# Kernel optimization log

Hardware: AMD Instinct MI355X
Metric: run time of the kernel (lower is better)

Reference implementation:

```python
import jax, jax.numpy as jnp
import numpy as np

B, T, N, D = 32, 50, 100, 4
E = N * (N - 1)
N_IN, N_HID, N_OUT = T * D, 256, 4


def _mlp(x, w1, b1, w2, b2):
    # Linear -> ReLU -> (dropout=0) -> Linear
    return jax.nn.relu(x @ w1 + b1) @ w2 + b2


def setup_inputs() -> dict:
    key = jax.random.key(0)
    ks = jax.random.split(key, 12)
    # fully-connected directed graph, no self loops
    idx = np.array([(i, j) for i in range(N) for j in range(N) if i != j], dtype=np.int64)
    recv, sendr = idx[:, 0], idx[:, 1]
    rec = jnp.asarray(np.eye(N, dtype=np.float32)[recv])    # [E, N]
    send = jnp.asarray(np.eye(N, dtype=np.float32)[sendr])  # [E, N]

    def lin(k, fan_in, fan_out):
        kw, kb = jax.random.split(k)
        w = jax.random.normal(kw, (fan_in, fan_out), jnp.float32) * 0.02
        b = jax.random.normal(kb, (fan_out,), jnp.float32) * 0.02
        return w, b

    x = jax.random.normal(ks[0], (B, T, N, D), jnp.float32)
    w1a, b1a = lin(ks[1], N_IN, N_HID)
    w1b, b1b = lin(ks[2], N_HID, N_HID)
    w2a, b2a = lin(ks[3], 2 * N_HID, N_HID)
    w2b, b2b = lin(ks[4], N_HID, N_HID)
    w3a, b3a = lin(ks[5], N_HID, N_HID)
    w3b, b3b = lin(ks[6], N_HID, N_HID)
    w4a, b4a = lin(ks[7], 3 * N_HID, N_HID)
    w4b, b4b = lin(ks[8], N_HID, N_HID)
    wo, bo = lin(ks[9], N_HID, N_OUT)
    return {"x": x, "rec": rec, "send": send,
            "w1a": w1a, "b1a": b1a, "w1b": w1b, "b1b": b1b,
            "w2a": w2a, "b2a": b2a, "w2b": w2b, "b2b": b2b,
            "w3a": w3a, "b3a": b3a, "w3b": w3b, "b3b": b3b,
            "w4a": w4a, "b4a": b4a, "w4b": w4b, "b4b": b4b,
            "wo": wo, "bo": bo}


def reference(x, rec, send,
              w1a, b1a, w1b, b1b,
              w2a, b2a, w2b, b2b,
              w3a, b3a, w3b, b3b,
              w4a, b4a, w4b, b4b,
              wo, bo):
    # [B, T, N, D] -> [B, N, T*D]
    h = jnp.transpose(x, (0, 2, 1, 3)).reshape(x.shape[0], x.shape[2], -1)
    h = _mlp(h, w1a, b1a, w1b, b1b)                       # [B, N, H]
    # v2e: gather receiver/sender node states to edges
    e = jnp.concatenate([jnp.einsum('en,bnh->beh', rec, h),
                         jnp.einsum('en,bnh->beh', send, h)], axis=2)  # [B, E, 2H]
    e = _mlp(e, w2a, b2a, w2b, b2b)                       # [B, E, H]
    x_skip = e
    # e2v: scatter edges back to nodes, normalize by n_nodes
    v = jnp.einsum('en,beh->bnh', rec, e) / e.shape[-2] * (e.shape[-2] / rec.shape[1])
    v = jnp.einsum('en,beh->bnh', rec, e) / rec.shape[1]  # incoming / incoming.size(1)=N
    v = _mlp(v, w3a, b3a, w3b, b3b)                       # [B, N, H]
    e2 = jnp.concatenate([jnp.einsum('en,bnh->beh', rec, v),
                          jnp.einsum('en,bnh->beh', send, v)], axis=2)  # [B, E, 2H]
    e2 = jnp.concatenate([e2, x_skip], axis=2)            # [B, E, 3H]
    e2 = _mlp(e2, w4a, b4a, w4b, b4b)                     # [B, E, H]
    return e2 @ wo + bo                                   # [B, E, n_out]
```

## Files before the change

### kernel.cpp

```cpp
#include <hip/hip_runtime.h>
#include <hip/hip_bf16.h>
#include <stdint.h>


typedef __attribute__((ext_vector_type(8))) short short8;
typedef __attribute__((ext_vector_type(4))) float float4v;
typedef __attribute__((ext_vector_type(4))) unsigned short ushort4v;

__device__ inline float bf2f(unsigned short u) {
    union { unsigned int i; float f; } v; v.i = ((unsigned int)u) << 16; return v.f;
}

#if __has_builtin(__builtin_amdgcn_cvt_pk_bf16_f32)
typedef __attribute__((ext_vector_type(2))) __bf16 bf16x2;
__device__ inline unsigned int f2bf_pk(float a, float b) {
    union { bf16x2 v; unsigned int u; } c;
    c.v = __builtin_amdgcn_cvt_pk_bf16_f32(a, b);
    return c.u;
}
__device__ inline unsigned short f2bf(float f) {
    return (unsigned short)(f2bf_pk(f, f) & 0xFFFFu);
}
#else
__device__ inline unsigned short f2bf(float f) {
    union { float f; unsigned int i; } v; v.f = f;
    unsigned int i = v.i;
    return (unsigned short)((i + 0x7FFFu + ((i >> 16) & 1u)) >> 16);
}
__device__ inline unsigned int f2bf_pk(float a, float b) {
    return (unsigned int)f2bf(a) | ((unsigned int)f2bf(b) << 16);
}
#endif

__global__ __launch_bounds__(256) void prep_kernel(
        const float* __restrict__ x,
        const float* __restrict__ w1a, const float* __restrict__ w1b,
        const float* __restrict__ w2a, const float* __restrict__ w2b,
        const float* __restrict__ w3a, const float* __restrict__ w3b,
        const float* __restrict__ w4a, const float* __restrict__ b4a,
        const float* __restrict__ w4b, const float* __restrict__ b4b,
        const float* __restrict__ wo,  const float* __restrict__ bo,
        const float* __restrict__ b2b,
        unsigned short* __restrict__ Wp1a, unsigned short* __restrict__ Wp1b,
        unsigned short* __restrict__ Wp2r, unsigned short* __restrict__ Wp2s,
        unsigned short* __restrict__ Wp2b, unsigned short* __restrict__ Wp3a,
        unsigned short* __restrict__ Wp3b, unsigned short* __restrict__ Wp4r,
        unsigned short* __restrict__ Wp4s, unsigned short* __restrict__ Wpz,
        unsigned short* __restrict__ Wfp, float* __restrict__ bfv,
        float* __restrict__ b4ap, float* __restrict__ b2bs,
        unsigned short* __restrict__ hin) {
    int bx = blockIdx.x;
    int tid = threadIdx.x;
    if (bx < 2272) {
        const float* W; unsigned short* Wp; int Kin; int b0;
        if      (bx <  224) { W = w1a;             Wp = Wp1a; Kin = 200; b0 = 0;    }
        else if (bx <  480) { W = w1b;             Wp = Wp1b; Kin = 256; b0 = 224;  }
        else if (bx <  736) { W = w2a;             Wp = Wp2r; Kin = 256; b0 = 480;  }
        else if (bx <  992) { W = w2a + 256 * 256; Wp = Wp2s; Kin = 256; b0 = 736;  }
        else if (bx < 1248) { W = w2b;             Wp = Wp2b; Kin = 256; b0 = 992;  }
        else if (bx < 1504) { W = w3a;             Wp = Wp3a; Kin = 256; b0 = 1248; }
        else if (bx < 1760) { W = w3b;             Wp = Wp3b; Kin = 256; b0 = 1504; }
        else if (bx < 2016) { W = w4a;             Wp = Wp4r; Kin = 256; b0 = 1760; }
        else                { W = w4a + 256 * 256; Wp = Wp4s; Kin = 256; b0 = 2016; }
        int idx = (bx - b0) * 256 + tid;
        int k = idx >> 8, n = idx & 255;
        unsigned short v = (k < Kin) ? f2bf(W[k * 256 + n]) : (unsigned short)0;
        Wp[((size_t)(k >> 5) * 256 + n) * 32 + (k & 31)] = v;
    } else if (bx < 2528) {
        int k = bx - 2272, c = tid;
        float s = 0.f;
        for (int t = 0; t < 256; ++t)
            s += w2b[k * 256 + t] * w4a[(size_t)(512 + t) * 256 + c];
        Wpz[((size_t)(k >> 5) * 256 + c) * 32 + (k & 31)] = f2bf(s);
    } else if (bx < 2530) {
        int k = tid;
        if (bx == 2528) {
            float a[4] = {0.f, 0.f, 0.f, 0.f};
            for (int c = 0; c < 256; ++c) {
                float wv = w4b[k * 256 + c];
                #pragma unroll
                for (int o = 0; o < 4; ++o) a[o] += wv * wo[c * 4 + o];
            }
            #pragma unroll
            for (int n = 0; n < 16; ++n)
                Wfp[(size_t)(k >> 5) * 512 + n * 32 + (k & 31)] =
                    (n < 4) ? f2bf(a[n]) : (unsigned short)0;
            if (k < 4) {
                float s = bo[k];
                for (int c = 0; c < 256; ++c) s += b4b[c] * wo[c * 4 + k];
                bfv[k] = s;
            }
        } else {
            float s = b4a[k];
            for (int t = 0; t < 256; ++t)
                s += b2b[t] * w4a[(size_t)(512 + t) * 256 + k];
            b4ap[k] = s;
            b2bs[k] = 0.99f * b2b[k];
        }
    } else {
        int idx = (bx - 2530) * 256 + tid;
        if (idx < 3200 * 224) {
            int row = idx / 224;
            int c = idx - row * 224;
            int b = row / 100, n = row - b * 100;
            unsigned short v = 0;
            if (c < 200) {
                int t = c >> 2, d = c & 3;
                v = f2bf(x[(((size_t)(b * 50 + t)) * 100 + n) * 4 + d]);
            }
            hin[(size_t)row * 224 + c] = v;
        }
    }
}

__global__ __launch_bounds__(256) void node_fusedA_kernel(
        const unsigned short* __restrict__ hin,
        const unsigned short* __restrict__ Wp1a, const float* __restrict__ b1a,
        const unsigned short* __restrict__ Wp1b, const float* __restrict__ b1b,
        const unsigned short* __restrict__ Wp2r, const float* __restrict__ b2a,
        const unsigned short* __restrict__ Wp2s,
        unsigned short* __restrict__ U, unsigned short* __restrict__ Hs) {
    __shared__ __align__(16) unsigned short t1s[16 * 264];
    __shared__ __align__(16) unsigned short hs2[16 * 264];
    const int m0 = blockIdx.x * 16;
    const int tid  = threadIdx.x;
    const int wave = tid >> 6;
    const int lane = tid & 63;
    const int l15  = lane & 15;
    const int quad = lane >> 4;
    const int n0   = wave * 64;
    const int koff = quad * 8;

    {
        float4v acc[4];
        #pragma unroll
        for (int ni = 0; ni < 4; ++ni) acc[ni] = (float4v)(0.0f);
        for (int kb = 0; kb < 7; ++kb) {
            short8 af = *(const short8*)(hin + (size_t)(m0 + l15) * 224 + kb * 32 + koff);
            short8 bf[4];
            #pragma unroll
            for (int ni = 0; ni < 4; ++ni)
                bf[ni] = *(const short8*)(Wp1a + ((size_t)kb * 256 + n0 + ni * 16 + l15) * 32 + koff);
            #pragma unroll
            for (int ni = 0; ni < 4; ++ni)
                acc[ni] = __builtin_amdgcn_mfma_f32_16x16x32_bf16(af, bf[ni], acc[ni], 0, 0, 0);
        }
        #pragma unroll
        for (int ni = 0; ni < 4; ++ni) {
            int col = n0 + ni * 16 + l15;
            float bv = b1a[col];
            #pragma unroll
            for (int r = 0; r < 4; ++r) {
                float v = acc[ni][r] + bv;
                v = v > 0.f ? v : 0.f;
                t1s[(quad * 4 + r) * 264 + col] = f2bf(v);
            }
        }
    }
    __syncthreads();

    {
        float4v acc[4];
        #pragma unroll
        for (int ni = 0; ni < 4; ++ni) acc[ni] = (float4v)(0.0f);
        for (int kb = 0; kb < 8; ++kb) {
            short8 af = *(const short8*)(&t1s[l15 * 264 + kb * 32 + koff]);
            short8 bf[4];
            #pragma unroll
            for (int ni = 0; ni < 4; ++ni)
                bf[ni] = *(const short8*)(Wp1b + ((size_t)kb * 256 + n0 + ni * 16 + l15) * 32 + koff);
            #pragma unroll
            for (int ni = 0; ni < 4; ++ni)
                acc[ni] = __builtin_amdgcn_mfma_f32_16x16x32_bf16(af, bf[ni], acc[ni], 0, 0, 0);
        }
        #pragma unroll
        for (int ni = 0; ni < 4; ++ni) {
            int col = n0 + ni * 16 + l15;
            float bv = b1b[col];
            #pragma unroll
            for (int r = 0; r < 4; ++r)
                hs2[(quad * 4 + r) * 264 + col] = f2bf(acc[ni][r] + bv);
        }
    }
    __syncthreads();

    {
        float4v aU[4], aH[4];
        #pragma unroll
        for (int ni = 0; ni < 4; ++ni) { aU[ni] = (float4v)(0.0f); aH[ni] = (float4v)(0.0f); }
        for (int kb = 0; kb < 8; ++kb) {
            short8 af = *(const short8*)(&hs2[l15 * 264 + kb * 32 + koff]);
            #pragma unroll
            for (int ni = 0; ni < 4; ++ni) {
                short8 bu = *(const short8*)(Wp2r + ((size_t)kb * 256 + n0 + ni * 16 + l15) * 32 + koff);
                short8 bh = *(const short8*)(Wp2s + ((size_t)kb * 256 + n0 + ni * 16 + l15) * 32 + koff);
                aU[ni] = __builtin_amdgcn_mfma_f32_16x16x32_bf16(af, bu, aU[ni], 0, 0, 0);
                aH[ni] = __builtin_amdgcn_mfma_f32_16x16x32_bf16(af, bh, aH[ni], 0, 0, 0);
            }
        }
        #pragma unroll
        for (int ni = 0; ni < 4; ++ni) {
            int col = n0 + ni * 16 + l15;
            float bv = b2a[col];
            #pragma unroll
            for (int r = 0; r < 4; ++r) {
                size_t o = (size_t)(m0 + quad * 4 + r) * 256 + col;
                U[o]  = f2bf(aU[ni][r] + bv);
                Hs[o] = f2bf(aH[ni][r]);
            }
        }
    }
}

__global__ __launch_bounds__(256) void node_fusedC_kernel(
        const unsigned short* __restrict__ Ssc,
        const unsigned short* __restrict__ Wp2b, const float* __restrict__ b2bs,
        const unsigned short* __restrict__ Wp3a, const float* __restrict__ b3a,
        const unsigned short* __restrict__ Wp3b, const float* __restrict__ b3b,
        const unsigned short* __restrict__ Wp4r, const float* __restrict__ b4ap,
        const unsigned short* __restrict__ Wp4s,
        unsigned short* __restrict__ C4, unsigned short* __restrict__ Vs) {
    __shared__ __align__(16) unsigned short buf0[16 * 264];
    __shared__ __align__(16) unsigned short buf1[16 * 264];
    const int m0 = blockIdx.x * 16;
    const int tid  = threadIdx.x;
    const int wave = tid >> 6;
    const int lane = tid & 63;
    const int l15  = lane & 15;
    const int quad = lane >> 4;
    const int n0   = wave * 64;
    const int koff = quad * 8;

    {
        float4v acc[4];
        #pragma unroll
        for (int ni = 0; ni < 4; ++ni) acc[ni] = (float4v)(0.0f);
        for (int kb = 0; kb < 8; ++kb) {
            short8 af = *(const short8*)(Ssc + (size_t)(m0 + l15) * 256 + kb * 32 + koff);
            short8 bf[4];
            #pragma unroll
            for (int ni = 0; ni < 4; ++ni)
                bf[ni] = *(const short8*)(Wp2b + ((size_t)kb * 256 + n0 + ni * 16 + l15) * 32 + koff);
            #pragma unroll
            for (int ni = 0; ni < 4; ++ni)
                acc[ni] = __builtin_amdgcn_mfma_f32_16x16x32_bf16(af, bf[ni], acc[ni], 0, 0, 0);
        }
        #pragma unroll
        for (int ni = 0; ni < 4; ++ni) {
            int col = n0 + ni * 16 + l15;
            float bv = b2bs[col];
            #pragma unroll
            for (int r = 0; r < 4; ++r)
                buf0[(quad * 4 + r) * 264 + col] = f2bf(acc[ni][r] + bv);
        }
    }
    __syncthreads();

    {
        float4v acc[4];
        #pragma unroll
        for (int ni = 0; ni < 4; ++ni) acc[ni] = (float4v)(0.0f);
        for (int kb = 0; kb < 8; ++kb) {
            short8 af = *(const short8*)(&buf0[l15 * 264 + kb * 32 + koff]);
            short8 bf[4];
            #pragma unroll
            for (int ni = 0; ni < 4; ++ni)
                bf[ni] = *(const short8*)(Wp3a + ((size_t)kb * 256 + n0 + ni * 16 + l15) * 32 + koff);
            #pragma unroll
            for (int ni = 0; ni < 4; ++ni)
                acc[ni] = __builtin_amdgcn_mfma_f32_16x16x32_bf16(af, bf[ni], acc[ni], 0, 0, 0);
        }
        #pragma unroll
        for (int ni = 0; ni < 4; ++ni) {
            int col = n0 + ni * 16 + l15;
            float bv = b3a[col];
            #pragma unroll
            for (int r = 0; r < 4; ++r) {
                float v = acc[ni][r] + bv;
                v = v > 0.f ? v : 0.f;
                buf1[(quad * 4 + r) * 264 + col] = f2bf(v);
            }
        }
    }
    __syncthreads();

    {
        float4v acc[4];
        #pragma unroll
        for (int ni = 0; ni < 4; ++ni) acc[ni] = (float4v)(0.0f);
        for (int kb = 0; kb < 8; ++kb) {
            short8 af = *(const short8*)(&buf1[l15 * 264 + kb * 32 + koff]);
            short8 bf[4];
            #pragma unroll
            for (int ni = 0; ni < 4; ++ni)
                bf[ni] = *(const short8*)(Wp3b + ((size_t)kb * 256 + n0 + ni * 16 + l15) * 32 + koff);
            #pragma unroll
            for (int ni = 0; ni < 4; ++ni)
                acc[ni] = __builtin_amdgcn_mfma_f32_16x16x32_bf16(af, bf[ni], acc[ni], 0, 0, 0);
        }
        __syncthreads();
        #pragma unroll
        for (int ni = 0; ni < 4; ++ni) {
            int col = n0 + ni * 16 + l15;
            float bv = b3b[col];
            #pragma unroll
            for (int r = 0; r < 4; ++r)
                buf0[(quad * 4 + r) * 264 + col] = f2bf(acc[ni][r] + bv);
        }
    }
    __syncthreads();

    {
        float4v aC[4], aV[4];
        #pragma unroll
        for (int ni = 0; ni < 4; ++ni) { aC[ni] = (float4v)(0.0f); aV[ni] = (float4v)(0.0f); }
        for (int kb = 0; kb < 8; ++kb) {
            short8 af = *(const short8*)(&buf0[l15 * 264 + kb * 32 + koff]);
            #pragma unroll
            for (int ni = 0; ni < 4; ++ni) {
                short8 bc = *(const short8*)(Wp4r + ((size_t)kb * 256 + n0 + ni * 16 + l15) * 32 + koff);
                short8 bv = *(const short8*)(Wp4s + ((size_t)kb * 256 + n0 + ni * 16 + l15) * 32 + koff);
                aC[ni] = __builtin_amdgcn_mfma_f32_16x16x32_bf16(af, bc, aC[ni], 0, 0, 0);
                aV[ni] = __builtin_amdgcn_mfma_f32_16x16x32_bf16(af, bv, aV[ni], 0, 0, 0);
            }
        }
        #pragma unroll
        for (int ni = 0; ni < 4; ++ni) {
            int col = n0 + ni * 16 + l15;
            float bv = b4ap[col];
            #pragma unroll
            for (int r = 0; r < 4; ++r) {
                size_t o = (size_t)(m0 + quad * 4 + r) * 256 + col;
                C4[o] = f2bf(aC[ni][r] + bv);
                Vs[o] = f2bf(aV[ni][r]);
            }
        }
    }
}

__global__ __launch_bounds__(256) void colsum_kernel(
        const unsigned short* __restrict__ U, const unsigned short* __restrict__ Hs,
        unsigned short* __restrict__ Ssc) {
    const int g = blockIdx.x;
    const int b = g / 100, i = g - b * 100;
    const int c = threadIdx.x;
    const float u = bf2f(U[(size_t)g * 256 + c]);
    const unsigned short* base = Hs + (size_t)b * 100 * 256 + c;
    float s = 0.f;
    #pragma unroll 4
    for (int j = 0; j < 100; ++j) {
        float v = u + bf2f(base[(size_t)j * 256]);
        s += (v > 0.f ? v : 0.f);
    }
    float vi = u + bf2f(base[(size_t)i * 256]);
    s -= (vi > 0.f ? vi : 0.f);
    Ssc[(size_t)g * 256 + c] = f2bf(s * 0.01f);
}

__global__ __launch_bounds__(512, 6) void edge_phaseB_kernel(
        const unsigned short* __restrict__ Hs, const unsigned short* __restrict__ Vs,
        const unsigned short* __restrict__ U, const unsigned short* __restrict__ C4,
        const unsigned short* __restrict__ Wpz, const unsigned short* __restrict__ Wfp,
        const float* __restrict__ bfv,
        float* __restrict__ out) {
    __shared__ __align__(16) unsigned short t2s[64 * 264];
    const int g = blockIdx.x, hb = blockIdx.y;
    const int b = g / 100, nr = g - b * 100;
    const int nrows = hb ? 49 : 50;
    const int k0 = hb * 50;
    const int tid  = threadIdx.x;
    const int wave = tid >> 6;
    const int lane = tid & 63;
    const int l15  = lane & 15;
    const int quad = lane >> 4;
    const int n0   = wave * 32;
    const int koff = quad * 8;

    {
        const int c = lane * 4;
        ushort4v uv = *(const ushort4v*)(U + (size_t)g * 256 + c);
        float u0 = bf2f(uv[0]), u1 = bf2f(uv[1]), u2 = bf2f(uv[2]), u3 = bf2f(uv[3]);
        for (int r = wave; r < 64; r += 8) {
            unsigned int p01 = 0, p23 = 0;
            if (r < nrows) {
                int k = k0 + r;
                int j = k + (k >= nr ? 1 : 0);
                ushort4v hv = *(const ushort4v*)(Hs + (size_t)(b * 100 + j) * 256 + c);
                float t0 = u0 + bf2f(hv[0]); t0 = t0 > 0.f ? t0 : 0.f;
                float t1 = u1 + bf2f(hv[1]); t1 = t1 > 0.f ? t1 : 0.f;
                float t2 = u2 + bf2f(hv[2]); t2 = t2 > 0.f ? t2 : 0.f;
                float t3 = u3 + bf2f(hv[3]); t3 = t3 > 0.f ? t3 : 0.f;
                p01 = f2bf_pk(t0, t1);
                p23 = f2bf_pk(t2, t3);
            }
            unsigned int* dst = (unsigned int*)(&t2s[r * 264 + c]);
            dst[0] = p01;
            dst[1] = p23;
        }
    }
    __syncthreads();

    float4v acc[4][2];
    #pragma unroll
    for (int mi = 0; mi < 4; ++mi) {
        acc[mi][0] = (float4v)(0.0f);
        acc[mi][1] = (float4v)(0.0f);
    }

    #pragma unroll 1
    for (int kb = 0; kb < 8; ++kb) {
        short8 bf0 = *(const short8*)(Wpz + ((size_t)kb * 256 + n0 + l15) * 32 + koff);
        short8 bf1 = *(const short8*)(Wpz + ((size_t)kb * 256 + n0 + 16 + l15) * 32 + koff);
        #pragma unroll
        for (int mi = 0; mi < 4; ++mi) {
            short8 af = *(const short8*)(&t2s[(mi * 16 + l15) * 264 + kb * 32 + koff]);
            acc[mi][0] = __builtin_amdgcn_mfma_f32_16x16x32_bf16(af, bf0, acc[mi][0], 0, 0, 0);
            acc[mi][1] = __builtin_amdgcn_mfma_f32_16x16x32_bf16(af, bf1, acc[mi][1], 0, 0, 0);
        }
    }
    __syncthreads();

    {
        float c4v0 = bf2f(C4[(size_t)g * 256 + n0 + l15]);
        float c4v1 = bf2f(C4[(size_t)g * 256 + n0 + 16 + l15]);
        #pragma unroll
        for (int mi = 0; mi < 4; ++mi) {
            #pragma unroll
            for (int r = 0; r < 4; ++r) {
                int row = mi * 16 + quad * 4 + r;
                int k = k0 + row;
                int j = (row < nrows) ? (k + (k >= nr ? 1 : 0)) : 0;
                const unsigned short* vsr = Vs + (size_t)(b * 100 + j) * 256;
                float z0 = c4v0 + bf2f(vsr[n0 + l15]) + acc[mi][0][r];
                float z1 = c4v1 + bf2f(vsr[n0 + 16 + l15]) + acc[mi][1][r];
                z0 = z0 > 0.f ? z0 : 0.f;
                z1 = z1 > 0.f ? z1 : 0.f;
                t2s[row * 264 + n0 + l15]      = f2bf(z0);
                t2s[row * 264 + n0 + 16 + l15] = f2bf(z1);
            }
        }
    }
    __syncthreads();

    if (wave < 4) {
        float4v pacc = (float4v)(0.0f);
        #pragma unroll
        for (int kb = 0; kb < 8; ++kb) {
            short8 za = *(const short8*)(&t2s[(wave * 16 + l15) * 264 + kb * 32 + koff]);
            short8 wb = *(const short8*)(Wfp + (size_t)kb * 512 + l15 * 32 + koff);
            pacc = __builtin_amdgcn_mfma_f32_16x16x32_bf16(za, wb, pacc, 0, 0, 0);
        }
        if (l15 < 4) {
            float bv = bfv[l15];
            #pragma unroll
            for (int r = 0; r < 4; ++r) {
                int row = wave * 16 + quad * 4 + r;
                if (row < nrows)
                    out[((size_t)b * 9900 + nr * 99 + k0 + row) * 4 + l15] = pacc[r] + bv;
            }
        }
    }
}

extern "C" void kernel_launch(void* const* d_in, const int* in_sizes, int n_in,
                              void* d_out, int out_size, void* d_ws, size_t ws_size,
                              hipStream_t stream) {
    const float* x   = (const float*)d_in[0];
    const float* w1a = (const float*)d_in[3];
    const float* b1a = (const float*)d_in[4];
    const float* w1b = (const float*)d_in[5];
    const float* b1b = (const float*)d_in[6];
    const float* w2a = (const float*)d_in[7];
    const float* b2a = (const float*)d_in[8];
    const float* w2b = (const float*)d_in[9];
    const float* b2b = (const float*)d_in[10];
    const float* w3a = (const float*)d_in[11];
    const float* b3a = (const float*)d_in[12];
    const float* w3b = (const float*)d_in[13];
    const float* b3b = (const float*)d_in[14];
    const float* w4a = (const float*)d_in[15];
    const float* b4a = (const float*)d_in[16];
    const float* w4b = (const float*)d_in[17];
    const float* b4b = (const float*)d_in[18];
    const float* wo  = (const float*)d_in[19];
    const float* bo  = (const float*)d_in[20];
    float* out = (float*)d_out;
    (void)in_sizes; (void)n_in; (void)out_size; (void)ws_size;

    char* ws = (char*)d_ws;
    size_t off = 0;
    auto alloc = [&](size_t bytes) {
        size_t o = off;
        off = (off + bytes + 255) & ~(size_t)255;
        return o;
    };
    const size_t SLOT_BF = (size_t)3200 * 256 * 2;
    unsigned short* S_U  = (unsigned short*)(ws + alloc(SLOT_BF));
    unsigned short* S_Hs = (unsigned short*)(ws + alloc(SLOT_BF));
    unsigned short* S_Vs = (unsigned short*)(ws + alloc(SLOT_BF));
    unsigned short* S_4  = (unsigned short*)(ws + alloc(SLOT_BF));
    unsigned short* Wp1a = (unsigned short*)(ws + alloc(224 * 256 * 2));
    unsigned short* Wp1b = (unsigned short*)(ws + alloc(256 * 256 * 2));
    unsigned short* Wp2r = (unsigned short*)(ws + alloc(256 * 256 * 2));
    unsigned short* Wp2s = (unsigned short*)(ws + alloc(256 * 256 * 2));
    unsigned short* Wp2b = (unsigned short*)(ws + alloc(256 * 256 * 2));
    unsigned short* Wp3a = (unsigned short*)(ws + alloc(256 * 256 * 2));
    unsigned short* Wp3b = (unsigned short*)(ws + alloc(256 * 256 * 2));
    unsigned short* Wp4r = (unsigned short*)(ws + alloc(256 * 256 * 2));
    unsigned short* Wp4s = (unsigned short*)(ws + alloc(256 * 256 * 2));
    unsigned short* Wpz  = (unsigned short*)(ws + alloc(256 * 256 * 2));
    unsigned short* Wfp  = (unsigned short*)(ws + alloc(8 * 16 * 32 * 2));
    float*          bfv  = (float*)(ws + alloc(4 * 4));
    float*          b4ap = (float*)(ws + alloc(256 * 4));
    float*          b2bs = (float*)(ws + alloc(256 * 4));

    unsigned short* hin = S_4;
    unsigned short* Ssc = S_4;
    unsigned short* C4  = S_4;

    hipLaunchKernelGGL(prep_kernel, dim3(5330), dim3(256), 0, stream,
                       x, w1a, w1b, w2a, w2b, w3a, w3b, w4a, b4a, w4b, b4b, wo, bo, b2b,
                       Wp1a, Wp1b, Wp2r, Wp2s, Wp2b, Wp3a, Wp3b, Wp4r, Wp4s, Wpz,
                       Wfp, bfv, b4ap, b2bs, hin);
    hipLaunchKernelGGL(node_fusedA_kernel, dim3(200), dim3(256), 0, stream,
                       hin, Wp1a, b1a, Wp1b, b1b, Wp2r, b2a, Wp2s, S_U, S_Hs);
    hipLaunchKernelGGL(colsum_kernel, dim3(3200), dim3(256), 0, stream, S_U, S_Hs, Ssc);
    hipLaunchKernelGGL(node_fusedC_kernel, dim3(200), dim3(256), 0, stream,
                       Ssc, Wp2b, b2bs, Wp3a, b3a, Wp3b, b3b, Wp4r, b4ap, Wp4s, C4, S_Vs);
    hipLaunchKernelGGL(edge_phaseB_kernel, dim3(3200, 2), dim3(512), 0, stream,
                       S_Hs, S_Vs, S_U, C4, Wpz, Wfp, bfv, out);
}
```

Baseline: 259.6 us.

## Double node-kernel wave count, vectorize colsum, pack bf16 conversions in edge kernel

The node MLP kernels now launch 8 waves per 16-row block, each owning 32 output columns instead of 64. This is meant to raise wave-level parallelism and latency hiding on a grid of only 200 blocks. The colsum kernel now processes four channels per thread with 64-bit vector loads and packed stores, using a quarter as many blocks. The edge kernel also converts its two ReLU outputs with a single packed bf16 conversion. Costs include more total loads of the shared A fragment and more waves competing for registers.

```diff
diff --git a/kernel.cpp b/kernel.cpp
--- a/kernel.cpp
+++ b/kernel.cpp
@@ -113,7 +113,7 @@
     }
 }
 
-__global__ __launch_bounds__(256) void node_fusedA_kernel(
+__global__ __launch_bounds__(512) void node_fusedA_kernel(
         const unsigned short* __restrict__ hin,
         const unsigned short* __restrict__ Wp1a, const float* __restrict__ b1a,
         const unsigned short* __restrict__ Wp1b, const float* __restrict__ b1b,
@@ -128,25 +128,22 @@
     const int lane = tid & 63;
     const int l15  = lane & 15;
     const int quad = lane >> 4;
-    const int n0   = wave * 64;
+    const int n0   = wave * 32;
     const int koff = quad * 8;
 
     {
-        float4v acc[4];
-        #pragma unroll
-        for (int ni = 0; ni < 4; ++ni) acc[ni] = (float4v)(0.0f);
+        float4v acc[2];
+        acc[0] = (float4v)(0.0f); acc[1] = (float4v)(0.0f);
         for (int kb = 0; kb < 7; ++kb) {
             short8 af = *(const short8*)(hin + (size_t)(m0 + l15) * 224 + kb * 32 + koff);
-            short8 bf[4];
-            #pragma unroll
-            for (int ni = 0; ni < 4; ++ni)
-                bf[ni] = *(const short8*)(Wp1a + ((size_t)kb * 256 + n0 + ni * 16 + l15) * 32 + koff);
-            #pragma unroll
-            for (int ni = 0; ni < 4; ++ni)
-                acc[ni] = __builtin_amdgcn_mfma_f32_16x16x32_bf16(af, bf[ni], acc[ni], 0, 0, 0);
-        }
-        #pragma unroll
-        for (int ni = 0; ni < 4; ++ni) {
+            #pragma unroll
+            for (int ni = 0; ni < 2; ++ni) {
+                short8 bf = *(const short8*)(Wp1a + ((size_t)kb * 256 + n0 + ni * 16 + l15) * 32 + koff);
+                acc[ni] = __builtin_amdgcn_mfma_f32_16x16x32_bf16(af, bf, acc[ni], 0, 0, 0);
+            }
+        }
+        #pragma unroll
+        for (int ni = 0; ni < 2; ++ni) {
             int col = n0 + ni * 16 + l15;
             float bv = b1a[col];
             #pragma unroll
@@ -160,21 +157,18 @@
     __syncthreads();
 
     {
-        float4v acc[4];
-        #pragma unroll
-        for (int ni = 0; ni < 4; ++ni) acc[ni] = (float4v)(0.0f);
+        float4v acc[2];
+        acc[0] = (float4v)(0.0f); acc[1] = (float4v)(0.0f);
         for (int kb = 0; kb < 8; ++kb) {
             short8 af = *(const short8*)(&t1s[l15 * 264 + kb * 32 + koff]);
-            short8 bf[4];
-            #pragma unroll
-            for (int ni = 0; ni < 4; ++ni)
-                bf[ni] = *(const short8*)(Wp1b + ((size_t)kb * 256 + n0 + ni * 16 + l15) * 32 + koff);
-            #pragma unroll
-            for (int ni = 0; ni < 4; ++ni)
-                acc[ni] = __builtin_amdgcn_mfma_f32_16x16x32_bf16(af, bf[ni], acc[ni], 0, 0, 0);
-        }
-        #pragma unroll
-        for (int ni = 0; ni < 4; ++ni) {
+            #pragma unroll
+            for (int ni = 0; ni < 2; ++ni) {
+                short8 bf = *(const short8*)(Wp1b + ((size_t)kb * 256 + n0 + ni * 16 + l15) * 32 + koff);
+                acc[ni] = __builtin_amdgcn_mfma_f32_16x16x32_bf16(af, bf, acc[ni], 0, 0, 0);
+            }
+        }
+        #pragma unroll
+        for (int ni = 0; ni < 2; ++ni) {
             int col = n0 + ni * 16 + l15;
             float bv = b1b[col];
             #pragma unroll
@@ -185,13 +179,13 @@
     __syncthreads();
 
     {
-        float4v aU[4], aH[4];
-        #pragma unroll
-        for (int ni = 0; ni < 4; ++ni) { aU[ni] = (float4v)(0.0f); aH[ni] = (float4v)(0.0f); }
+        float4v aU[2], aH[2];
+        aU[0] = (float4v)(0.0f); aU[1] = (float4v)(0.0f);
+        aH[0] = (float4v)(0.0f); aH[1] = (float4v)(0.0f);
         for (int kb = 0; kb < 8; ++kb) {
             short8 af = *(const short8*)(&hs2[l15 * 264 + kb * 32 + koff]);
             #pragma unroll
-            for (int ni = 0; ni < 4; ++ni) {
+            for (int ni = 0; ni < 2; ++ni) {
                 short8 bu = *(const short8*)(Wp2r + ((size_t)kb * 256 + n0 + ni * 16 + l15) * 32 + koff);
                 short8 bh = *(const short8*)(Wp2s + ((size_t)kb * 256 + n0 + ni * 16 + l15) * 32 + koff);
                 aU[ni] = __builtin_amdgcn_mfma_f32_16x16x32_bf16(af, bu, aU[ni], 0, 0, 0);
@@ -199,7 +193,7 @@
             }
         }
         #pragma unroll
-        for (int ni = 0; ni < 4; ++ni) {
+        for (int ni = 0; ni < 2; ++ni) {
             int col = n0 + ni * 16 + l15;
             float bv = b2a[col];
             #pragma unroll
@@ -212,7 +206,7 @@
     }
 }
 
-__global__ __launch_bounds__(256) void node_fusedC_kernel(
+__global__ __launch_bounds__(512) void node_fusedC_kernel(
         const unsigned short* __restrict__ Ssc,
         const unsigned short* __restrict__ Wp2b, const float* __restrict__ b2bs,
         const unsigned short* __restrict__ Wp3a, const float* __restrict__ b3a,
@@ -228,25 +222,22 @@
     const int lane = tid & 63;
     const int l15  = lane & 15;
     const int quad = lane >> 4;
-    const int n0   = wave * 64;
+    const int n0   = wave * 32;
     const int koff = quad * 8;
 
     {
-        float4v acc[4];
-        #pragma unroll
-        for (int ni = 0; ni < 4; ++ni) acc[ni] = (float4v)(0.0f);
+        float4v acc[2];
+        acc[0] = (float4v)(0.0f); acc[1] = (float4v)(0.0f);
         for (int kb = 0; kb < 8; ++kb) {
             short8 af = *(const short8*)(Ssc + (size_t)(m0 + l15) * 256 + kb * 32 + koff);
-            short8 bf[4];
-            #pragma unroll
-            for (int ni = 0; ni < 4; ++ni)
-                bf[ni] = *(const short8*)(Wp2b + ((size_t)kb * 256 + n0 + ni * 16 + l15) * 32 + koff);
-            #pragma unroll
-            for (int ni = 0; ni < 4; ++ni)
-                acc[ni] = __builtin_amdgcn_mfma_f32_16x16x32_bf16(af, bf[ni], acc[ni], 0, 0, 0);
-        }
-        #pragma unroll
-        for (int ni = 0; ni < 4; ++ni) {
+            #pragma unroll
+            for (int ni = 0; ni < 2; ++ni) {
+                short8 bf = *(const short8*)(Wp2b + ((size_t)kb * 256 + n0 + ni * 16 + l15) * 32 + koff);
+                acc[ni] = __builtin_amdgcn_mfma_f32_16x16x32_bf16(af, bf, acc[ni], 0, 0, 0);
+            }
+        }
+        #pragma unroll
+        for (int ni = 0; ni < 2; ++ni) {
             int col = n0 + ni * 16 + l15;
             float bv = b2bs[col];
             #pragma unroll
@@ -257,21 +248,18 @@
     __syncthreads();
 
     {
-        float4v acc[4];
-        #pragma unroll
-        for (int ni = 0; ni < 4; ++ni) acc[ni] = (float4v)(0.0f);
+        float4v acc[2];
+        acc[0] = (float4v)(0.0f); acc[1] = (float4v)(0.0f);
         for (int kb = 0; kb < 8; ++kb) {
             short8 af = *(const short8*)(&buf0[l15 * 264 + kb * 32 + koff]);
-            short8 bf[4];
-            #pragma unroll
-            for (int ni = 0; ni < 4; ++ni)
-                bf[ni] = *(const short8*)(Wp3a + ((size_t)kb * 256 + n0 + ni * 16 + l15) * 32 + koff);
-            #pragma unroll
-            for (int ni = 0; ni < 4; ++ni)
-                acc[ni] = __builtin_amdgcn_mfma_f32_16x16x32_bf16(af, bf[ni], acc[ni], 0, 0, 0);
-        }
-        #pragma unroll
-        for (int ni = 0; ni < 4; ++ni) {
+            #pragma unroll
+            for (int ni = 0; ni < 2; ++ni) {
+                short8 bf = *(const short8*)(Wp3a + ((size_t)kb * 256 + n0 + ni * 16 + l15) * 32 + koff);
+                acc[ni] = __builtin_amdgcn_mfma_f32_16x16x32_bf16(af, bf, acc[ni], 0, 0, 0);
+            }
+        }
+        #pragma unroll
+        for (int ni = 0; ni < 2; ++ni) {
             int col = n0 + ni * 16 + l15;
             float bv = b3a[col];
             #pragma unroll
@@ -285,22 +273,19 @@
     __syncthreads();
 
     {
-        float4v acc[4];
-        #pragma unroll
-        for (int ni = 0; ni < 4; ++ni) acc[ni] = (float4v)(0.0f);
+        float4v acc[2];
+        acc[0] = (float4v)(0.0f); acc[1] = (float4v)(0.0f);
         for (int kb = 0; kb < 8; ++kb) {
             short8 af = *(const short8*)(&buf1[l15 * 264 + kb * 32 + koff]);
-            short8 bf[4];
-            #pragma unroll
-            for (int ni = 0; ni < 4; ++ni)
-                bf[ni] = *(const short8*)(Wp3b + ((size_t)kb * 256 + n0 + ni * 16 + l15) * 32 + koff);
-            #pragma unroll
-            for (int ni = 0; ni < 4; ++ni)
-                acc[ni] = __builtin_amdgcn_mfma_f32_16x16x32_bf16(af, bf[ni], acc[ni], 0, 0, 0);
+            #pragma unroll
+            for (int ni = 0; ni < 2; ++ni) {
+                short8 bf = *(const short8*)(Wp3b + ((size_t)kb * 256 + n0 + ni * 16 + l15) * 32 + koff);
+                acc[ni] = __builtin_amdgcn_mfma_f32_16x16x32_bf16(af, bf, acc[ni], 0, 0, 0);
+            }
         }
         __syncthreads();
         #pragma unroll
-        for (int ni = 0; ni < 4; ++ni) {
+        for (int ni = 0; ni < 2; ++ni) {
             int col = n0 + ni * 16 + l15;
             float bv = b3b[col];
             #pragma unroll
@@ -311,13 +296,13 @@
     __syncthreads();
 
     {
-        float4v aC[4], aV[4];
-        #pragma unroll
-        for (int ni = 0; ni < 4; ++ni) { aC[ni] = (float4v)(0.0f); aV[ni] = (float4v)(0.0f); }
+        float4v aC[2], aV[2];
+        aC[0] = (float4v)(0.0f); aC[1] = (float4v)(0.0f);
+        aV[0] = (float4v)(0.0f); aV[1] = (float4v)(0.0f);
         for (int kb = 0; kb < 8; ++kb) {
             short8 af = *(const short8*)(&buf0[l15 * 264 + kb * 32 + koff]);
             #pragma unroll
-            for (int ni = 0; ni < 4; ++ni) {
+            for (int ni = 0; ni < 2; ++ni) {
                 short8 bc = *(const short8*)(Wp4r + ((size_t)kb * 256 + n0 + ni * 16 + l15) * 32 + koff);
                 short8 bv = *(const short8*)(Wp4s + ((size_t)kb * 256 + n0 + ni * 16 + l15) * 32 + koff);
                 aC[ni] = __builtin_amdgcn_mfma_f32_16x16x32_bf16(af, bc, aC[ni], 0, 0, 0);
@@ -325,7 +310,7 @@
             }
         }
         #pragma unroll
-        for (int ni = 0; ni < 4; ++ni) {
+        for (int ni = 0; ni < 2; ++ni) {
             int col = n0 + ni * 16 + l15;
             float bv = b4ap[col];
             #pragma unroll
@@ -341,20 +326,31 @@
 __global__ __launch_bounds__(256) void colsum_kernel(
         const unsigned short* __restrict__ U, const unsigned short* __restrict__ Hs,
         unsigned short* __restrict__ Ssc) {
-    const int g = blockIdx.x;
+    const int g = blockIdx.x * 4 + (threadIdx.x >> 6);
     const int b = g / 100, i = g - b * 100;
-    const int c = threadIdx.x;
-    const float u = bf2f(U[(size_t)g * 256 + c]);
+    const int c = (threadIdx.x & 63) * 4;
+    ushort4v uv = *(const ushort4v*)(U + (size_t)g * 256 + c);
+    const float u0 = bf2f(uv[0]), u1 = bf2f(uv[1]), u2 = bf2f(uv[2]), u3 = bf2f(uv[3]);
     const unsigned short* base = Hs + (size_t)b * 100 * 256 + c;
-    float s = 0.f;
+    float s0 = 0.f, s1 = 0.f, s2 = 0.f, s3 = 0.f;
     #pragma unroll 4
     for (int j = 0; j < 100; ++j) {
-        float v = u + bf2f(base[(size_t)j * 256]);
-        s += (v > 0.f ? v : 0.f);
-    }
-    float vi = u + bf2f(base[(size_t)i * 256]);
-    s -= (vi > 0.f ? vi : 0.f);
-    Ssc[(size_t)g * 256 + c] = f2bf(s * 0.01f);
+        ushort4v hv = *(const ushort4v*)(base + (size_t)j * 256);
+        float v0 = u0 + bf2f(hv[0]); s0 += (v0 > 0.f ? v0 : 0.f);
+        float v1 = u1 + bf2f(hv[1]); s1 += (v1 > 0.f ? v1 : 0.f);
+        float v2 = u2 + bf2f(hv[2]); s2 += (v2 > 0.f ? v2 : 0.f);
+        float v3 = u3 + bf2f(hv[3]); s3 += (v3 > 0.f ? v3 : 0.f);
+    }
+    {
+        ushort4v hv = *(const ushort4v*)(base + (size_t)i * 256);
+        float v0 = u0 + bf2f(hv[0]); s0 -= (v0 > 0.f ? v0 : 0.f);
+        float v1 = u1 + bf2f(hv[1]); s1 -= (v1 > 0.f ? v1 : 0.f);
+        float v2 = u2 + bf2f(hv[2]); s2 -= (v2 > 0.f ? v2 : 0.f);
+        float v3 = u3 + bf2f(hv[3]); s3 -= (v3 > 0.f ? v3 : 0.f);
+    }
+    unsigned int* dst = (unsigned int*)(Ssc + (size_t)g * 256 + c);
+    dst[0] = f2bf_pk(s0 * 0.01f, s1 * 0.01f);
+    dst[1] = f2bf_pk(s2 * 0.01f, s3 * 0.01f);
 }
 
 __global__ __launch_bounds__(512, 6) void edge_phaseB_kernel(
@@ -435,8 +431,9 @@
                 float z1 = c4v1 + bf2f(vsr[n0 + 16 + l15]) + acc[mi][1][r];
                 z0 = z0 > 0.f ? z0 : 0.f;
                 z1 = z1 > 0.f ? z1 : 0.f;
-                t2s[row * 264 + n0 + l15]      = f2bf(z0);
-                t2s[row * 264 + n0 + 16 + l15] = f2bf(z1);
+                unsigned int zp = f2bf_pk(z0, z1);
+                t2s[row * 264 + n0 + l15]      = (unsigned short)zp;
+                t2s[row * 264 + n0 + 16 + l15] = (unsigned short)(zp >> 16);
             }
         }
     }
@@ -522,10 +519,10 @@
                        x, w1a, w1b, w2a, w2b, w3a, w3b, w4a, b4a, w4b, b4b, wo, bo, b2b,
                        Wp1a, Wp1b, Wp2r, Wp2s, Wp2b, Wp3a, Wp3b, Wp4r, Wp4s, Wpz,
                        Wfp, bfv, b4ap, b2bs, hin);
-    hipLaunchKernelGGL(node_fusedA_kernel, dim3(200), dim3(256), 0, stream,
+    hipLaunchKernelGGL(node_fusedA_kernel, dim3(200), dim3(512), 0, stream,
                        hin, Wp1a, b1a, Wp1b, b1b, Wp2r, b2a, Wp2s, S_U, S_Hs);
-    hipLaunchKernelGGL(colsum_kernel, dim3(3200), dim3(256), 0, stream, S_U, S_Hs, Ssc);
-    hipLaunchKernelGGL(node_fusedC_kernel, dim3(200), dim3(256), 0, stream,
+    hipLaunchKernelGGL(colsum_kernel, dim3(800), dim3(256), 0, stream, S_U, S_Hs, Ssc);
+    hipLaunchKernelGGL(node_fusedC_kernel, dim3(200), dim3(512), 0, stream,
                        Ssc, Wp2b, b2bs, Wp3a, b3a, Wp3b, b3b, Wp4r, b4ap, Wp4s, C4, S_Vs);
     hipLaunchKernelGGL(edge_phaseB_kernel, dim3(3200, 2), dim3(512), 0, stream,
                        S_Hs, S_Vs, S_U, C4, Wpz, Wfp, bfv, out);
```

Result: no change. 256.2 us (-1.3%).
